# Kernel optimization log

Hardware: AMD Instinct MI355X
Metric: run time of the kernel (lower is better)

The kernel has to match this reference:

```python
import jax, jax.numpy as jnp
import numpy as np

EPS = 1e-8
SLOPE = 0.2  # default negative_slope in VNLinearLeakyReLU
N_KNN = 4
GS_EPS = 1e-6
NOISE_SCALE = 0.1


def vn_linear(x, W):
    # x: (B, Cin, 3, ...), W: (Cout, Cin) -> (B, Cout, 3, ...)
    return jnp.einsum('oc,bc...->bo...', W, x)


def vn_linear_leaky_relu(x, Wf, Wd):
    p = vn_linear(x, Wf)
    d = vn_linear(x, Wd)
    dot = jnp.sum(p * d, axis=2, keepdims=True)
    d2 = jnp.sum(d * d, axis=2, keepdims=True)
    neg = p - (dot / (d2 + EPS)) * d
    return SLOPE * p + (1.0 - SLOPE) * jnp.where(dot >= 0, p, neg)


def vn_max_pool(x, Wd):
    # pools over the last axis using a learned direction
    d = vn_linear(x, Wd)
    dot = jnp.sum(x * d, axis=2, keepdims=True)          # (B,C,1,...,N)
    idx = jnp.argmax(dot, axis=-1)                       # (B,C,1,...)
    idx = jnp.broadcast_to(idx, x.shape[:-1])[..., None]
    return jnp.take_along_axis(x, idx, axis=-1)[..., 0]


def get_graph_feature(x, knn):
    # x: (B, C, 3, N) -> (B, 2C, 3, N, knn)
    B, C, _, N = x.shape
    xf = x.reshape(B, 3 * C, N)
    xx = jnp.sum(xf * xf, axis=1)                        # (B,N)
    inner = jnp.einsum('bdn,bdm->bnm', xf, xf)           # (B,N,N)
    neg_dist = 2.0 * inner - xx[:, :, None] - xx[:, None, :]
    _, idx = jax.lax.top_k(neg_dist, knn)                # (B,N,knn)
    pts = x.transpose(0, 3, 1, 2)                        # (B,N,C,3)
    nbrs = pts[jnp.arange(B)[:, None, None], idx]        # (B,N,knn,C,3)
    ctr = jnp.broadcast_to(pts[:, :, None], nbrs.shape)
    feat = jnp.concatenate([nbrs - ctr, ctr], axis=3)    # (B,N,knn,2C,3)
    return feat.transpose(0, 3, 4, 1, 2)


def batched_gram_schmidt_3d(M):
    # orthonormalize the columns of (B,3,3)
    def nrm(v):
        return v / (jnp.linalg.norm(v, axis=-1, keepdims=True) + EPS)
    v1, v2, v3 = M[:, :, 0], M[:, :, 1], M[:, :, 2]
    e1 = nrm(v1)
    u2 = v2 - jnp.sum(e1 * v2, -1, keepdims=True) * e1
    e2 = nrm(u2)
    u3 = v3 - jnp.sum(e1 * v3, -1, keepdims=True) * e1 - jnp.sum(e2 * v3, -1, keepdims=True) * e2
    e3 = nrm(u3)
    return jnp.stack([e1, e2, e3], axis=-1)


def setup_inputs() -> dict:
    key = jax.random.key(0)
    ks = jax.random.split(key, 10)
    b, n, d_node, d_edge, kk, dim = 4, 2048, 2, 4, 4, 32  # dim = 96 // 3
    return {
        'node_features': jax.random.normal(ks[0], (b, n, 3, d_node), jnp.float32),
        'edge_features': jax.random.normal(ks[1], (b, n, n, d_edge), jnp.float32),
        'idx': jnp.arange(b, dtype=jnp.int32),
        'k': kk,
        'W1f': jax.random.normal(ks[2], (dim, 2 * d_node), jnp.float32) * 0.3,
        'W1d': jax.random.normal(ks[3], (dim, 2 * d_node), jnp.float32) * 0.3,
        'Wp1': jax.random.normal(ks[4], (dim, dim), jnp.float32) * 0.1,
        'Wp3': jax.random.normal(ks[5], (dim, dim), jnp.float32) * 0.1,
        'Wh2': jax.random.normal(ks[6], (3, dim), jnp.float32) * 0.1,
        'z': jax.random.normal(ks[7], (b, kk, n, 3, d_node), jnp.float32) * NOISE_SCALE,
        'gs_noise': jax.random.normal(ks[8], (b, kk, 3, 3), jnp.float32),
    }


def reference(node_features, edge_features, idx, k, W1f, W1d, Wp1, Wp3, Wh2, z, gs_noise):
    b, n, _, d = node_features.shape
    # replicate k times and add invariant noise (fixed_noise=False path)
    x = jnp.broadcast_to(node_features[:, None], (b, k, n, 3, d)) + z
    x = x.reshape(b * k, n, 3, d).transpose(0, 3, 2, 1)   # (bk, d, 3, n)
    g = get_graph_feature(x, N_KNN)                       # (bk, 2d, 3, n, knn)
    h = vn_linear_leaky_relu(g, W1f, W1d)                 # (bk, dim, 3, n, knn)
    x1 = vn_max_pool(h, Wp1)                              # (bk, dim, 3, n)
    pooled = vn_max_pool(x1, Wp3)                         # (bk, dim, 3)
    pk = vn_linear(pooled, Wh2)                           # (bk, 3, 3)
    pk = pk.transpose(0, 2, 1).reshape(b, k, 3, 3)
    pk = pk + GS_EPS * gs_noise
    R = batched_gram_schmidt_3d(pk.reshape(b * k, 3, 3))
    det = jnp.linalg.det(R)                               # SO3 sign fix on column 0
    R = R.at[:, :, 0].multiply(det[:, None])
    return R.reshape(b, k, 3, 3)
```

## Files before the change

kernel.cpp:

```cpp
#include <hip/hip_runtime.h>
#include <math.h>

#define EPSF    1e-8f
#define SLOPEF  0.2f
#define GS_EPSF 1e-6f

#define NB   4
#define KZ   4
#define BKT  16
#define NPT  2048
#define DIM  32

#define COMP(v,kk) ((kk)==0?(v).x:(kk)==1?(v).y:(kk)==2?(v).z:(v).w)

typedef float f2 __attribute__((ext_vector_type(2)));

__device__ __forceinline__ void fma4(float4& acc, float s, const float4& v) {
  acc.x = fmaf(s, v.x, acc.x); acc.y = fmaf(s, v.y, acc.y);
  acc.z = fmaf(s, v.z, acc.z); acc.w = fmaf(s, v.w, acc.w);
}

__global__ __launch_bounds__(256) void prep_coords(
    const float* __restrict__ node, const float* __restrict__ z,
    const float* __restrict__ Wp1, const float* __restrict__ Wp3,
    float4* __restrict__ pts, float* __restrict__ ptsPf,
    float4* __restrict__ wpk) {
  if (blockIdx.x == 0) {
    int i = threadIdx.x;
    int og = i & 7, c = i >> 3;
    wpk[i]       = make_float4(Wp1[og * 32 + c], Wp1[(og + 8) * 32 + c],
                               Wp1[(og + 16) * 32 + c], Wp1[(og + 24) * 32 + c]);
    wpk[256 + i] = make_float4(Wp3[og * 32 + c], Wp3[(og + 8) * 32 + c],
                               Wp3[(og + 16) * 32 + c], Wp3[(og + 24) * 32 + c]);
  }
  int t = blockIdx.x * 256 + threadIdx.x;
  if (t >= BKT * NPT) return;
  int bk = t >> 11, n = t & (NPT - 1);
  int b = bk >> 2, kz = bk & 3;
  const float2* np2 = (const float2*)(node + (size_t)(b * NPT + n) * 6);
  const float2* zp2 = (const float2*)(z + (size_t)((b * KZ + kz) * NPT + n) * 6);
  float ch[6];
#pragma unroll
  for (int j = 0; j < 3; ++j) {
    float2 a = np2[j], c = zp2[j];
    ch[j]     = a.x + c.x;
    ch[3 + j] = a.y + c.y;
  }
  float xx = 0.f;
#pragma unroll
  for (int h = 0; h < 6; ++h) xx = fmaf(ch[h], ch[h], xx);
  pts[(size_t)t * 2 + 0] = make_float4(ch[0], ch[1], ch[2], ch[3]);
  pts[(size_t)t * 2 + 1] = make_float4(ch[4], ch[5], xx, 0.f);
  size_t pbase = (size_t)(t >> 1) * 16 + (t & 1);
#pragma unroll
  for (int c = 0; c < 6; ++c) ptsPf[pbase + c * 2] = ch[c];
  ptsPf[pbase + 12] = xx;
}

__device__ __forceinline__ void ins3m(float s, int j,
    float& v0, float& v1, float& v2, int& i0, int& i1, int& i2) {
  bool c0 = s > v0, c1 = s > v1, c2 = s > v2;
  float nv0 = fmaxf(v0, s);
  float nv1 = __builtin_amdgcn_fmed3f(v0, v1, s);
  float nv2 = __builtin_amdgcn_fmed3f(v1, v2, s);
  i2 = c1 ? i1 : (c2 ? j : i2);
  i1 = c0 ? i0 : (c1 ? j : i1);
  i0 = c0 ? j : i0;
  v0 = nv0; v1 = nv1; v2 = nv2;
}

__device__ __forceinline__ void ce(float& vx, int& ix, float& vy, int& iy) {
  float av = vx, bv = vy; int ai = ix, bi = iy;
  bool sw = (bv > av) || (bv == av && bi < ai);
  vx = sw ? bv : av; vy = sw ? av : bv;
  ix = sw ? bi : ai; iy = sw ? ai : bi;
}

template <bool SELF>
__device__ __forceinline__ void scan128P(const float4* __restrict__ pp4,
    int j0, int q, const float4 qa, const float4 qb,
    float& v0, float& v1, float& v2, int& i0, int& i1, int& i2) {
  f2 qx = {qa.x, qa.x}, qy = {qa.y, qa.y}, qz = {qa.z, qa.z}, qw = {qa.w, qa.w};
  f2 qu = {qb.x, qb.x}, qv = {qb.y, qb.y}, mh = {-0.5f, -0.5f};
#pragma unroll 2
  for (int pr = 0; pr < 64; ++pr) {
    float4 L0 = pp4[pr * 4 + 0], L1 = pp4[pr * 4 + 1];
    float4 L2 = pp4[pr * 4 + 2], L3 = pp4[pr * 4 + 3];
    f2 ax = {L0.x, L0.y}, ay = {L0.z, L0.w};
    f2 az = {L1.x, L1.y}, aw = {L1.z, L1.w};
    f2 au = {L2.x, L2.y}, av = {L2.z, L2.w};
    f2 Xa = {L3.x, L3.y};
    f2 sa = qx * ax;
    sa = __builtin_elementwise_fma(qy, ay, sa);
    sa = __builtin_elementwise_fma(qz, az, sa);
    sa = __builtin_elementwise_fma(qw, aw, sa);
    sa = __builtin_elementwise_fma(qu, au, sa);
    sa = __builtin_elementwise_fma(qv, av, sa);
    sa = __builtin_elementwise_fma(mh, Xa, sa);
    int jb = j0 + 2 * pr;
    float s0 = sa.x, s1 = sa.y;
    if (SELF) {
      if (jb + 0 == q) s0 = -INFINITY;
      if (jb + 1 == q) s1 = -INFINITY;
    }
    ins3m(s0, jb + 0, v0, v1, v2, i0, i1, i2);
    ins3m(s1, jb + 1, v0, v1, v2, i0, i1, i2);
  }
}

__global__ __launch_bounds__(1024, 8) void knn_kernel(
    const float4* __restrict__ pts, const float4* __restrict__ ptsP,
    int4* __restrict__ knn4) {
  __shared__ float4 lv[16][64];
  __shared__ int4   li[16][64];
  int lane = threadIdx.x & 63;
  int w = threadIdx.x >> 6;
  int bk = blockIdx.x >> 5, qg = blockIdx.x & 31;
  int base = bk * NPT;
  int q = qg * 64 + lane;
  float4 qa = pts[(size_t)(base + q) * 2 + 0];
  float4 qb = pts[(size_t)(base + q) * 2 + 1];
  int j0 = __builtin_amdgcn_readfirstlane(w * 128);
  const float4* pp4 = ptsP + ((size_t)(base + j0) >> 1) * 4;
  float v0 = -INFINITY, v1 = -INFINITY, v2 = -INFINITY;
  int   i0 = 0x7fffffff, i1 = 0x7fffffff, i2 = 0x7fffffff;
  if (w == (qg >> 1)) scan128P<true >(pp4, j0, q, qa, qb, v0, v1, v2, i0, i1, i2);
  else                scan128P<false>(pp4, j0, q, qa, qb, v0, v1, v2, i0, i1, i2);
  lv[w][lane] = make_float4(v0, v1, v2, -INFINITY);
  li[w][lane] = make_int4(i0, i1, i2, 0x7fffffff);
  __syncthreads();
#pragma unroll
  for (int str = 8; str >= 1; str >>= 1) {
    if (w < str) {
      float4 av = lv[w][lane];        int4 ai = li[w][lane];
      float4 bv = lv[w + str][lane];  int4 bi = li[w + str][lane];
      float a0 = av.x, a1 = av.y, a2 = av.z, a3 = av.w;
      int   c0 = ai.x, c1 = ai.y, c2 = ai.z, c3 = ai.w;
      float s4 = bv.w, s5 = bv.z, s6 = bv.y, s7 = bv.x;
      int   t4 = bi.w, t5 = bi.z, t6 = bi.y, t7 = bi.x;
      ce(a0, c0, s4, t4); ce(a1, c1, s5, t5);
      ce(a2, c2, s6, t6); ce(a3, c3, s7, t7);
      ce(a0, c0, a2, c2); ce(a1, c1, a3, c3);
      ce(a0, c0, a1, c1); ce(a2, c2, a3, c3);
      lv[w][lane] = make_float4(a0, a1, a2, a3);
      li[w][lane] = make_int4(c0, c1, c2, c3);
    }
    __syncthreads();
  }
  if (w == 0) {
    int4 r = li[0][lane];
    knn4[base + q] = make_int4(q, r.x, r.y, r.z);
  }
}

__global__ __launch_bounds__(128) void feature_kernel(
    const float4* __restrict__ pts, const int4* __restrict__ knn4,
    const float* __restrict__ W1f, const float* __restrict__ W1d,
    const float4* __restrict__ wpk,
    float4* __restrict__ partials) {
  __shared__ float4 hlds[16][97];
  __shared__ float  dlds[16][33];
  int p = threadIdx.x >> 3;
  int og = threadIdx.x & 7;
  int bk = blockIdx.x >> 7, pb = blockIdx.x & 127;
  int n = (pb << 4) | p;
  int base = bk * NPT;
  float4 ca = pts[(size_t)(base + n) * 2 + 0], cbv = pts[(size_t)(base + n) * 2 + 1];
  float ct[6] = {ca.x, ca.y, ca.z, ca.w, cbv.x, cbv.y};
  float w1f[4][4], w1d[4][4];
#pragma unroll
  for (int m = 0; m < 4; ++m) {
    float4 wf = reinterpret_cast<const float4*>(W1f)[og + 8 * m];
    float4 wd = reinterpret_cast<const float4*>(W1d)[og + 8 * m];
    w1f[m][0] = wf.x; w1f[m][1] = wf.y; w1f[m][2] = wf.z; w1f[m][3] = wf.w;
    w1d[m][0] = wd.x; w1d[m][1] = wd.y; w1d[m][2] = wd.z; w1d[m][3] = wd.w;
  }
  int4 nb = knn4[base + n];
  int nbi[4] = {nb.x, nb.y, nb.z, nb.w};
  float h[4][4][3];
#pragma unroll
  for (int kk = 0; kk < 4; ++kk) {
    int mi = nbi[kk];
    float4 A = pts[(size_t)(base + mi) * 2 + 0], B = pts[(size_t)(base + mi) * 2 + 1];
    float nc[6] = {A.x, A.y, A.z, A.w, B.x, B.y};
    float G[4][3];
#pragma unroll
    for (int j = 0; j < 3; ++j) {
      G[0][j] = nc[j] - ct[j];
      G[1][j] = nc[3 + j] - ct[3 + j];
      G[2][j] = ct[j];
      G[3][j] = ct[3 + j];
    }
#pragma unroll
    for (int m = 0; m < 4; ++m) {
      float pvv[3], dv[3];
#pragma unroll
      for (int j = 0; j < 3; ++j) {
        float a = 0.f, dd = 0.f;
#pragma unroll
        for (int c = 0; c < 4; ++c) { a = fmaf(w1f[m][c], G[c][j], a); dd = fmaf(w1d[m][c], G[c][j], dd); }
        pvv[j] = a; dv[j] = dd;
      }
      float dot = pvv[0] * dv[0] + pvv[1] * dv[1] + pvv[2] * dv[2];
      float d2  = dv[0] * dv[0] + dv[1] * dv[1] + dv[2] * dv[2];
      float fac = dot / (d2 + EPSF);
#pragma unroll
      for (int j = 0; j < 3; ++j) {
        float negj = pvv[j] - fac * dv[j];
        float sel = (dot >= 0.f) ? pvv[j] : negj;
        h[m][kk][j] = SLOPEF * pvv[j] + (1.f - SLOPEF) * sel;
      }
    }
  }
#pragma unroll
  for (int m = 0; m < 4; ++m)
#pragma unroll
    for (int j = 0; j < 3; ++j)
      hlds[p][(og + 8 * m) * 3 + j] =
          make_float4(h[m][0][j], h[m][1][j], h[m][2][j], h[m][3][j]);
  __syncthreads();
  float4 d1j0[4], d1j1[4], d1j2[4];
#pragma unroll
  for (int m = 0; m < 4; ++m) {
    d1j0[m] = make_float4(0.f, 0.f, 0.f, 0.f);
    d1j1[m] = make_float4(0.f, 0.f, 0.f, 0.f);
    d1j2[m] = make_float4(0.f, 0.f, 0.f, 0.f);
  }
  for (int c = 0; c < 32; ++c) {
    float4 wv = wpk[c * 8 + og];
    float4 h0 = hlds[p][c * 3 + 0];
    float4 h1 = hlds[p][c * 3 + 1];
    float4 h2 = hlds[p][c * 3 + 2];
#pragma unroll
    for (int m = 0; m < 4; ++m) {
      float wm = COMP(wv, m);
      fma4(d1j0[m], wm, h0);
      fma4(d1j1[m], wm, h1);
      fma4(d1j2[m], wm, h2);
    }
  }
  float x1[4][3];
#pragma unroll
  for (int m = 0; m < 4; ++m) {
    float best = -INFINITY;
    float xa = 0.f, xb = 0.f, xc = 0.f;
#pragma unroll
    for (int kk = 0; kk < 4; ++kk) {
      float dt = h[m][kk][0] * COMP(d1j0[m], kk)
               + h[m][kk][1] * COMP(d1j1[m], kk)
               + h[m][kk][2] * COMP(d1j2[m], kk);
      if (dt > best) { best = dt; xa = h[m][kk][0]; xb = h[m][kk][1]; xc = h[m][kk][2]; }
    }
    x1[m][0] = xa; x1[m][1] = xb; x1[m][2] = xc;
  }
  __syncthreads();
#pragma unroll
  for (int m = 0; m < 4; ++m)
    hlds[p][og + 8 * m] = make_float4(x1[m][0], x1[m][1], x1[m][2], 0.f);
  __syncthreads();
  float d3[4][3] = {};
  for (int c = 0; c < 32; ++c) {
    float4 wv = wpk[256 + c * 8 + og];
    float4 xv = hlds[p][c];
#pragma unroll
    for (int m = 0; m < 4; ++m) {
      float wm = COMP(wv, m);
      d3[m][0] = fmaf(wm, xv.x, d3[m][0]);
      d3[m][1] = fmaf(wm, xv.y, d3[m][1]);
      d3[m][2] = fmaf(wm, xv.z, d3[m][2]);
    }
  }
#pragma unroll
  for (int m = 0; m < 4; ++m)
    dlds[p][og + 8 * m] = x1[m][0] * d3[m][0] + x1[m][1] * d3[m][1] + x1[m][2] * d3[m][2];
  __syncthreads();
  if (threadIdx.x < 32) {
    int o = threadIdx.x;
    float bd = -INFINITY; int wp_ = 0;
#pragma unroll
    for (int p2 = 0; p2 < 16; ++p2) {
      float dv = dlds[p2][o];
      if (dv > bd) { bd = dv; wp_ = p2; }
    }
    float4 xv = hlds[wp_][o];
    partials[(((size_t)(bk * 32 + o)) << 7) | pb] = make_float4(xv.x, xv.y, xv.z, bd);
  }
}

__global__ __launch_bounds__(256) void poolhead_kernel(
    const float4* __restrict__ partials, const float* __restrict__ Wh2,
    const float* __restrict__ gs, float* __restrict__ out) {
  __shared__ float pl[DIM][3];
  int bk = blockIdx.x;
  int o = threadIdx.x >> 3, tg = threadIdx.x & 7;
  const float4* pp = partials + (((size_t)(bk * 32 + o)) << 7);
  float best = -INFINITY; int bp = 0x7fffffff;
  for (int t = 0; t < 16; ++t) {
    int pb = t * 8 + tg;
    float v = pp[pb].w;
    if (v > best) { best = v; bp = pb; }
  }
#pragma unroll
  for (int off = 1; off < 8; off <<= 1) {
    float ov = __shfl_xor(best, off, 8);
    int   op = __shfl_xor(bp, off, 8);
    if (ov > best || (ov == best && op < bp)) { best = ov; bp = op; }
  }
  if (tg == 0) {
    float4 xv = pp[bp];
    pl[o][0] = xv.x; pl[o][1] = xv.y; pl[o][2] = xv.z;
  }
  __syncthreads();
  if (threadIdx.x == 0) {
    float M[3][3];
#pragma unroll
    for (int oo = 0; oo < 3; ++oo) {
      float a0 = 0.f, a1 = 0.f, a2 = 0.f;
      for (int c = 0; c < 32; ++c) {
        float w = Wh2[oo * 32 + c];
        a0 = fmaf(w, pl[c][0], a0);
        a1 = fmaf(w, pl[c][1], a1);
        a2 = fmaf(w, pl[c][2], a2);
      }
      M[0][oo] = a0 + GS_EPSF * gs[bk * 9 + 0 * 3 + oo];
      M[1][oo] = a1 + GS_EPSF * gs[bk * 9 + 1 * 3 + oo];
      M[2][oo] = a2 + GS_EPSF * gs[bk * 9 + 2 * 3 + oo];
    }
    float e1[3], e2[3], e3[3], u[3];
    float nn = sqrtf(M[0][0] * M[0][0] + M[1][0] * M[1][0] + M[2][0] * M[2][0]) + EPSF;
#pragma unroll
    for (int r = 0; r < 3; ++r) e1[r] = M[r][0] / nn;
    float d12 = e1[0] * M[0][1] + e1[1] * M[1][1] + e1[2] * M[2][1];
#pragma unroll
    for (int r = 0; r < 3; ++r) u[r] = M[r][1] - d12 * e1[r];
    nn = sqrtf(u[0] * u[0] + u[1] * u[1] + u[2] * u[2]) + EPSF;
#pragma unroll
    for (int r = 0; r < 3; ++r) e2[r] = u[r] / nn;
    float d13 = e1[0] * M[0][2] + e1[1] * M[1][2] + e1[2] * M[2][2];
    float d23 = e2[0] * M[0][2] + e2[1] * M[1][2] + e2[2] * M[2][2];
#pragma unroll
    for (int r = 0; r < 3; ++r) u[r] = M[r][2] - d13 * e1[r] - d23 * e2[r];
    nn = sqrtf(u[0] * u[0] + u[1] * u[1] + u[2] * u[2]) + EPSF;
#pragma unroll
    for (int r = 0; r < 3; ++r) e3[r] = u[r] / nn;
    float det = e1[0] * (e2[1] * e3[2] - e2[2] * e3[1])
              - e1[1] * (e2[0] * e3[2] - e2[2] * e3[0])
              + e1[2] * (e2[0] * e3[1] - e2[1] * e3[0]);
#pragma unroll
    for (int r = 0; r < 3; ++r) {
      out[bk * 9 + r * 3 + 0] = e1[r] * det;
      out[bk * 9 + r * 3 + 1] = e2[r];
      out[bk * 9 + r * 3 + 2] = e3[r];
    }
  }
}

extern "C" void kernel_launch(void* const* d_in, const int* in_sizes, int n_in,
                              void* d_out, int out_size, void* d_ws, size_t ws_size,
                              hipStream_t stream) {
  (void)in_sizes; (void)n_in; (void)out_size; (void)ws_size;
  const float* node = (const float*)d_in[0];
  const float* W1f = (const float*)d_in[4];
  const float* W1d = (const float*)d_in[5];
  const float* Wp1 = (const float*)d_in[6];
  const float* Wp3 = (const float*)d_in[7];
  const float* Wh2 = (const float*)d_in[8];
  const float* z   = (const float*)d_in[9];
  const float* gs  = (const float*)d_in[10];

  float4* pts      = (float4*)d_ws;
  int4*   knn4     = (int4*)(pts + (size_t)BKT * NPT * 2);
  float4* partials = (float4*)(knn4 + (size_t)BKT * NPT);
  float4* wpk      = partials + (size_t)BKT * 32 * 128;
  float4* ptsP     = wpk + 512;
  float*  out      = (float*)d_out;

  prep_coords    <<<BKT * NPT / 256, 256, 0, stream>>>(node, z, Wp1, Wp3, pts,
                                                       (float*)ptsP, wpk);
  knn_kernel     <<<BKT * 32, 1024, 0, stream>>>(pts, ptsP, knn4);
  feature_kernel <<<BKT * 128, 128, 0, stream>>>(pts, knn4, W1f, W1d, wpk, partials);
  poolhead_kernel<<<BKT, 256, 0, stream>>>(partials, Wh2, gs, out);
}
```

Before: 79.84 us.

## Process two queries per thread in kNN scan to reuse candidate loads

Each thread in the kNN kernel now handles two query points, so every candidate point loaded from global memory is reused for two distance computations. The grid is halved to match. The shared-memory merge switches to a structure-of-arrays top-3 layout with a smaller 3-element merge network. This trades higher register pressure (the min-waves hint is dropped from launch bounds) and fewer blocks in flight for halved load traffic per distance.

```diff
diff --git a/kernel.cpp b/kernel.cpp
--- a/kernel.cpp
+++ b/kernel.cpp
@@ -77,11 +77,16 @@
 }
 
 template <bool SELF>
-__device__ __forceinline__ void scan128P(const float4* __restrict__ pp4,
-    int j0, int q, const float4 qa, const float4 qb,
-    float& v0, float& v1, float& v2, int& i0, int& i1, int& i2) {
-  f2 qx = {qa.x, qa.x}, qy = {qa.y, qa.y}, qz = {qa.z, qa.z}, qw = {qa.w, qa.w};
-  f2 qu = {qb.x, qb.x}, qv = {qb.y, qb.y}, mh = {-0.5f, -0.5f};
+__device__ __forceinline__ void scan128Q2(const float4* __restrict__ pp4,
+    int j0, int q0, int q1,
+    const float4 qa0, const float4 qb0, const float4 qa1, const float4 qb1,
+    float& a0, float& a1, float& a2, int& ia0, int& ia1, int& ia2,
+    float& b0, float& b1, float& b2, int& ib0, int& ib1, int& ib2) {
+  f2 q0x = {qa0.x, qa0.x}, q0y = {qa0.y, qa0.y}, q0z = {qa0.z, qa0.z}, q0w = {qa0.w, qa0.w};
+  f2 q0u = {qb0.x, qb0.x}, q0v = {qb0.y, qb0.y};
+  f2 q1x = {qa1.x, qa1.x}, q1y = {qa1.y, qa1.y}, q1z = {qa1.z, qa1.z}, q1w = {qa1.w, qa1.w};
+  f2 q1u = {qb1.x, qb1.x}, q1v = {qb1.y, qb1.y};
+  f2 mh = {-0.5f, -0.5f};
 #pragma unroll 2
   for (int pr = 0; pr < 64; ++pr) {
     float4 L0 = pp4[pr * 4 + 0], L1 = pp4[pr * 4 + 1];
@@ -90,66 +95,86 @@
     f2 az = {L1.x, L1.y}, aw = {L1.z, L1.w};
     f2 au = {L2.x, L2.y}, av = {L2.z, L2.w};
     f2 Xa = {L3.x, L3.y};
-    f2 sa = qx * ax;
-    sa = __builtin_elementwise_fma(qy, ay, sa);
-    sa = __builtin_elementwise_fma(qz, az, sa);
-    sa = __builtin_elementwise_fma(qw, aw, sa);
-    sa = __builtin_elementwise_fma(qu, au, sa);
-    sa = __builtin_elementwise_fma(qv, av, sa);
-    sa = __builtin_elementwise_fma(mh, Xa, sa);
+    f2 s0 = q0x * ax;
+    s0 = __builtin_elementwise_fma(q0y, ay, s0);
+    s0 = __builtin_elementwise_fma(q0z, az, s0);
+    s0 = __builtin_elementwise_fma(q0w, aw, s0);
+    s0 = __builtin_elementwise_fma(q0u, au, s0);
+    s0 = __builtin_elementwise_fma(q0v, av, s0);
+    s0 = __builtin_elementwise_fma(mh, Xa, s0);
+    f2 s1 = q1x * ax;
+    s1 = __builtin_elementwise_fma(q1y, ay, s1);
+    s1 = __builtin_elementwise_fma(q1z, az, s1);
+    s1 = __builtin_elementwise_fma(q1w, aw, s1);
+    s1 = __builtin_elementwise_fma(q1u, au, s1);
+    s1 = __builtin_elementwise_fma(q1v, av, s1);
+    s1 = __builtin_elementwise_fma(mh, Xa, s1);
     int jb = j0 + 2 * pr;
-    float s0 = sa.x, s1 = sa.y;
+    float sA0 = s0.x, sA1 = s0.y, sB0 = s1.x, sB1 = s1.y;
     if (SELF) {
-      if (jb + 0 == q) s0 = -INFINITY;
-      if (jb + 1 == q) s1 = -INFINITY;
-    }
-    ins3m(s0, jb + 0, v0, v1, v2, i0, i1, i2);
-    ins3m(s1, jb + 1, v0, v1, v2, i0, i1, i2);
-  }
-}
-
-__global__ __launch_bounds__(1024, 8) void knn_kernel(
+      if (jb + 0 == q0) sA0 = -INFINITY;
+      if (jb + 1 == q0) sA1 = -INFINITY;
+      if (jb + 0 == q1) sB0 = -INFINITY;
+      if (jb + 1 == q1) sB1 = -INFINITY;
+    }
+    ins3m(sA0, jb + 0, a0, a1, a2, ia0, ia1, ia2);
+    ins3m(sA1, jb + 1, a0, a1, a2, ia0, ia1, ia2);
+    ins3m(sB0, jb + 0, b0, b1, b2, ib0, ib1, ib2);
+    ins3m(sB1, jb + 1, b0, b1, b2, ib0, ib1, ib2);
+  }
+}
+
+__global__ __launch_bounds__(1024) void knn_kernel(
     const float4* __restrict__ pts, const float4* __restrict__ ptsP,
     int4* __restrict__ knn4) {
-  __shared__ float4 lv[16][64];
-  __shared__ int4   li[16][64];
+  __shared__ float lv0[16][128], lv1[16][128], lv2[16][128];
+  __shared__ int   li0[16][128], li1[16][128], li2[16][128];
   int lane = threadIdx.x & 63;
   int w = threadIdx.x >> 6;
-  int bk = blockIdx.x >> 5, qg = blockIdx.x & 31;
+  int bk = blockIdx.x >> 4, qg = blockIdx.x & 15;
   int base = bk * NPT;
-  int q = qg * 64 + lane;
-  float4 qa = pts[(size_t)(base + q) * 2 + 0];
-  float4 qb = pts[(size_t)(base + q) * 2 + 1];
+  int q0 = qg * 128 + lane;
+  int q1 = q0 + 64;
+  float4 qa0 = pts[(size_t)(base + q0) * 2 + 0];
+  float4 qb0 = pts[(size_t)(base + q0) * 2 + 1];
+  float4 qa1 = pts[(size_t)(base + q1) * 2 + 0];
+  float4 qb1 = pts[(size_t)(base + q1) * 2 + 1];
   int j0 = __builtin_amdgcn_readfirstlane(w * 128);
   const float4* pp4 = ptsP + ((size_t)(base + j0) >> 1) * 4;
-  float v0 = -INFINITY, v1 = -INFINITY, v2 = -INFINITY;
-  int   i0 = 0x7fffffff, i1 = 0x7fffffff, i2 = 0x7fffffff;
-  if (w == (qg >> 1)) scan128P<true >(pp4, j0, q, qa, qb, v0, v1, v2, i0, i1, i2);
-  else                scan128P<false>(pp4, j0, q, qa, qb, v0, v1, v2, i0, i1, i2);
-  lv[w][lane] = make_float4(v0, v1, v2, -INFINITY);
-  li[w][lane] = make_int4(i0, i1, i2, 0x7fffffff);
+  float a0 = -INFINITY, a1 = -INFINITY, a2 = -INFINITY;
+  int   ia0 = 0x7fffffff, ia1 = 0x7fffffff, ia2 = 0x7fffffff;
+  float b0 = -INFINITY, b1 = -INFINITY, b2 = -INFINITY;
+  int   ib0 = 0x7fffffff, ib1 = 0x7fffffff, ib2 = 0x7fffffff;
+  if (w == qg) scan128Q2<true >(pp4, j0, q0, q1, qa0, qb0, qa1, qb1,
+                                a0, a1, a2, ia0, ia1, ia2, b0, b1, b2, ib0, ib1, ib2);
+  else         scan128Q2<false>(pp4, j0, q0, q1, qa0, qb0, qa1, qb1,
+                                a0, a1, a2, ia0, ia1, ia2, b0, b1, b2, ib0, ib1, ib2);
+  lv0[w][lane] = a0; lv1[w][lane] = a1; lv2[w][lane] = a2;
+  li0[w][lane] = ia0; li1[w][lane] = ia1; li2[w][lane] = ia2;
+  lv0[w][lane + 64] = b0; lv1[w][lane + 64] = b1; lv2[w][lane + 64] = b2;
+  li0[w][lane + 64] = ib0; li1[w][lane + 64] = ib1; li2[w][lane + 64] = ib2;
   __syncthreads();
 #pragma unroll
   for (int str = 8; str >= 1; str >>= 1) {
     if (w < str) {
-      float4 av = lv[w][lane];        int4 ai = li[w][lane];
-      float4 bv = lv[w + str][lane];  int4 bi = li[w + str][lane];
-      float a0 = av.x, a1 = av.y, a2 = av.z, a3 = av.w;
-      int   c0 = ai.x, c1 = ai.y, c2 = ai.z, c3 = ai.w;
-      float s4 = bv.w, s5 = bv.z, s6 = bv.y, s7 = bv.x;
-      int   t4 = bi.w, t5 = bi.z, t6 = bi.y, t7 = bi.x;
-      ce(a0, c0, s4, t4); ce(a1, c1, s5, t5);
-      ce(a2, c2, s6, t6); ce(a3, c3, s7, t7);
-      ce(a0, c0, a2, c2); ce(a1, c1, a3, c3);
-      ce(a0, c0, a1, c1); ce(a2, c2, a3, c3);
-      lv[w][lane] = make_float4(a0, a1, a2, a3);
-      li[w][lane] = make_int4(c0, c1, c2, c3);
+#pragma unroll
+      for (int h = 0; h < 2; ++h) {
+        int qi = lane + 64 * h;
+        float x0 = lv0[w][qi], x1 = lv1[w][qi], x2 = lv2[w][qi];
+        int   j0_ = li0[w][qi], j1_ = li1[w][qi], j2_ = li2[w][qi];
+        float y0 = lv0[w + str][qi], y1 = lv1[w + str][qi], y2 = lv2[w + str][qi];
+        int   k0_ = li0[w + str][qi], k1_ = li1[w + str][qi], k2_ = li2[w + str][qi];
+        ce(x0, j0_, y2, k2_); ce(x1, j1_, y1, k1_); ce(x2, j2_, y0, k0_);
+        ce(x0, j0_, x1, j1_); ce(x1, j1_, x2, j2_); ce(x0, j0_, x1, j1_);
+        lv0[w][qi] = x0; lv1[w][qi] = x1; lv2[w][qi] = x2;
+        li0[w][qi] = j0_; li1[w][qi] = j1_; li2[w][qi] = j2_;
+      }
     }
     __syncthreads();
   }
   if (w == 0) {
-    int4 r = li[0][lane];
-    knn4[base + q] = make_int4(q, r.x, r.y, r.z);
+    knn4[base + q0] = make_int4(q0, li0[0][lane], li1[0][lane], li2[0][lane]);
+    knn4[base + q1] = make_int4(q1, li0[0][lane + 64], li1[0][lane + 64], li2[0][lane + 64]);
   }
 }
 
@@ -377,7 +402,7 @@
 
   prep_coords    <<<BKT * NPT / 256, 256, 0, stream>>>(node, z, Wp1, Wp3, pts,
                                                        (float*)ptsP, wpk);
-  knn_kernel     <<<BKT * 32, 1024, 0, stream>>>(pts, ptsP, knn4);
+  knn_kernel     <<<BKT * 16, 1024, 0, stream>>>(pts, ptsP, knn4);
   feature_kernel <<<BKT * 128, 128, 0, stream>>>(pts, knn4, W1f, W1d, wpk, partials);
   poolhead_kernel<<<BKT, 256, 0, stream>>>(partials, Wh2, gs, out);
 }
```

After: 86.98 us. 1.09x slower.
